# Optimization experiments

Hardware: AMD Instinct MI355X
Metric: run time of the kernel (lower is better)

## Reference

```python
import jax, jax.numpy as jnp
import numpy as np

N_NODES = 50000
N_EDGES = 800000
IN_FEATS = 256
OUT_FEATS = 64


def setup_inputs() -> dict:
    key = jax.random.key(0)
    k1, k2, k3, k4 = jax.random.split(key, 4)
    feat = jax.random.normal(k1, (N_NODES, IN_FEATS), dtype=jnp.float32)
    src = jax.random.randint(k2, (N_EDGES,), 0, N_NODES, dtype=jnp.int32)
    dst = jax.random.randint(k3, (N_EDGES,), 0, N_NODES, dtype=jnp.int32)
    # Glorot-uniform like DGL's GraphConv weight init
    limit = float(np.sqrt(6.0 / (IN_FEATS + OUT_FEATS)))
    W = jax.random.uniform(k4, (IN_FEATS, OUT_FEATS), dtype=jnp.float32,
                           minval=-limit, maxval=limit)
    b = jnp.zeros((OUT_FEATS,), dtype=jnp.float32)
    return {"feat": feat, "src": src, "dst": dst, "W": W, "b": b}


def reference(feat, src, dst, W, b):
    n = feat.shape[0]
    ones = jnp.ones_like(src, dtype=feat.dtype)
    out_deg = jax.ops.segment_sum(ones, src, num_segments=n)
    in_deg = jax.ops.segment_sum(ones, dst, num_segments=n)
    # norm='both': deg^{-1/2}, degrees clamped to min 1 (allow_zero_in_degree)
    norm_src = jax.lax.rsqrt(jnp.maximum(out_deg, 1.0))   # [N]
    norm_dst = jax.lax.rsqrt(jnp.maximum(in_deg, 1.0))    # [N]
    # in_feats > out_feats -> apply weight before aggregation (DGL fast path)
    h = (feat * norm_src[:, None]) @ W                    # [N, out]
    agg = jax.ops.segment_sum(h[src], dst, num_segments=n)  # SpMM: sum messages at dst
    rst = agg * norm_dst[:, None] + b
    return jax.nn.sigmoid(rst)
```

## Files before the change

### kernel.cpp

```cpp
#include <hip/hip_runtime.h>
#include <hip/hip_bf16.h>
#include <math.h>

#define N_NODES 50000
#define N_EDGES 800000
#define IN_F 256
#define OUT_F 64

#define BKT 256
#define NB 196
#define CAP 6144
#define PARTA_BLOCKS 400
#define EPB (N_EDGES / PARTA_BLOCKS)
#define GEMM_BM 32

typedef __attribute__((ext_vector_type(8))) short bf16x8;
typedef __attribute__((ext_vector_type(4))) float f32x4;

__device__ __forceinline__ ushort f2bf(float x) {
    __hip_bfloat16 b = __float2bfloat16(x);
    return *reinterpret_cast<ushort*>(&b);
}
__device__ __forceinline__ float bf_lo(uint v) { return __uint_as_float(v << 16); }
__device__ __forceinline__ float bf_hi(uint v) { return __uint_as_float(v & 0xffff0000u); }

__global__ __launch_bounds__(256) void prep_kernel(int* __restrict__ bcnt,
                                                   const float* __restrict__ W,
                                                   ushort* __restrict__ Wpk) {
    const int tid = threadIdx.x;
    if (blockIdx.x == 0) {
        for (int i = tid; i < 2 * NB; i += 256) bcnt[i] = 0;
    } else {
        const int gid = (blockIdx.x - 1) * 256 + tid;
        const int lane = gid & 63;
        const int ct = (gid >> 6) & 3;
        const int step = gid >> 8;
        const int kg = lane >> 4;
        const int n = lane & 15;
        const float* base = W + (size_t)(step * 32 + kg * 8) * OUT_F + ct * 16 + n;
        union { ushort u[8]; uint4 v; } pk;
        #pragma unroll
        for (int j = 0; j < 8; ++j) pk.u[j] = f2bf(base[(size_t)j * OUT_F]);
        ((uint4*)Wpk)[gid] = pk.v;
    }
}

__global__ __launch_bounds__(512) void partA_kernel(const int* __restrict__ src,
                                                    const int* __restrict__ dst,
                                                    int* __restrict__ bcntD,
                                                    int* __restrict__ bcntS,
                                                    uint* __restrict__ pairsD,
                                                    ushort* __restrict__ srcloc) {
    __shared__ int2 ed[EPB];
    __shared__ uint stgD[EPB];
    __shared__ ushort stgS[EPB];
    __shared__ int lcntD[256], lcntS[256];
    __shared__ int ldofD[256], ldofS[256];
    __shared__ int lbaseD[NB], lbaseS[NB];
    __shared__ int wtotD[4], wtotS[4];
    const int tid = threadIdx.x;
    const int n4 = EPB / 4;

    for (int i = tid; i < 256; i += 512) { lcntD[i] = 0; lcntS[i] = 0; }
    __syncthreads();

    const int4* t4 = (const int4*)(dst + (size_t)blockIdx.x * EPB);
    const int4* s4 = (const int4*)(src + (size_t)blockIdx.x * EPB);
    for (int i = tid; i < n4; i += 512) {
        const int4 d = t4[i];
        const int4 s = s4[i];
        ed[4 * i + 0] = (int2){d.x, s.x};
        ed[4 * i + 1] = (int2){d.y, s.y};
        ed[4 * i + 2] = (int2){d.z, s.z};
        ed[4 * i + 3] = (int2){d.w, s.w};
        atomicAdd(&lcntD[d.x >> 8], 1); atomicAdd(&lcntS[s.x >> 8], 1);
        atomicAdd(&lcntD[d.y >> 8], 1); atomicAdd(&lcntS[s.y >> 8], 1);
        atomicAdd(&lcntD[d.z >> 8], 1); atomicAdd(&lcntS[s.z >> 8], 1);
        atomicAdd(&lcntD[d.w >> 8], 1); atomicAdd(&lcntS[s.w >> 8], 1);
    }
    __syncthreads();

    for (int i = tid; i < NB; i += 512) {
        const int cD = lcntD[i];
        lbaseD[i] = cD ? atomicAdd(&bcntD[i], cD) : 0;
        const int cS = lcntS[i];
        lbaseS[i] = cS ? atomicAdd(&bcntS[i], cS) : 0;
    }

    if (tid < 256) {
        const int lane = tid & 63;
        const int wave = tid >> 6;
        const int vD = lcntD[tid], vS = lcntS[tid];
        int iD = vD, iS = vS;
        #pragma unroll
        for (int d = 1; d < 64; d <<= 1) {
            const int uD = __shfl_up(iD, d, 64);
            const int uS = __shfl_up(iS, d, 64);
            if (lane >= d) { iD += uD; iS += uS; }
        }
        if (lane == 63) { wtotD[wave] = iD; wtotS[wave] = iS; }
        ldofD[tid] = iD - vD;
        ldofS[tid] = iS - vS;
    }
    __syncthreads();
    if (tid < 256) {
        const int wave = tid >> 6;
        int woD = 0, woS = 0;
        #pragma unroll
        for (int w = 0; w < 4; ++w)
            if (w < wave) { woD += wtotD[w]; woS += wtotS[w]; }
        ldofD[tid] += woD;
        ldofS[tid] += woS;
        lcntD[tid] = 0;
        lcntS[tid] = 0;
    }
    __syncthreads();

    for (int i = tid; i < EPB; i += 512) {
        const int2 e = ed[i];
        int bx = e.x >> 8;
        int pos = atomicAdd(&lcntD[bx], 1);
        stgD[ldofD[bx] + pos] =
            ((uint)bx << 24) | ((uint)(e.x & 255) << 16) | (uint)e.y;
        bx = e.y >> 8;
        pos = atomicAdd(&lcntS[bx], 1);
        stgS[ldofS[bx] + pos] = (ushort)((bx << 8) | (e.y & 255));
    }
    __syncthreads();

    for (int i = tid; i < EPB; i += 512) {
        const uint pv = stgD[i];
        const int bD = (int)(pv >> 24);
        pairsD[(size_t)bD * CAP + lbaseD[bD] + (i - ldofD[bD])] = pv & 0xFFFFFFu;
        const ushort sv = stgS[i];
        const int bS = sv >> 8;
        srcloc[(size_t)bS * CAP + lbaseS[bS] + (i - ldofS[bS])] = (ushort)(sv & 255u);
    }
}

__global__ __launch_bounds__(1024) void bucket_kernel(const ushort* __restrict__ srcloc,
                                                      const int* __restrict__ bcntS,
                                                      float* __restrict__ normS,
                                                      const uint* __restrict__ pairsD,
                                                      const int* __restrict__ bcntD,
                                                      uint* __restrict__ ptrdeg,
                                                      ushort* __restrict__ sorted_src) {
    __shared__ int cnt[BKT];
    __shared__ int loff[BKT];
    __shared__ int wtot[4];
    const int bb = blockIdx.x;
    const int tid = threadIdx.x;
    const int node = bb * BKT + tid;

    if (tid < BKT) cnt[tid] = 0;
    __syncthreads();
    const int nS = bcntS[bb];
    const ushort* sp = srcloc + (size_t)bb * CAP;
    for (int i = tid; i < nS; i += 1024) atomicAdd(&cnt[sp[i]], 1);
    __syncthreads();
    if (tid < BKT && node < N_NODES)
        normS[node] = rsqrtf(fmaxf((float)cnt[tid], 1.0f));
    __syncthreads();

    if (tid < BKT) cnt[tid] = 0;
    __syncthreads();
    const int nD = bcntD[bb];
    const uint* pb = pairsD + (size_t)bb * CAP;
    for (int i = tid; i < nD; i += 1024) atomicAdd(&cnt[(pb[i] >> 16) & 255u], 1);
    __syncthreads();

    if (tid < BKT) {
        const int lane = tid & 63;
        const int wave = tid >> 6;
        const int v = cnt[tid];
        int incl = v;
        #pragma unroll
        for (int d = 1; d < 64; d <<= 1) {
            int u = __shfl_up(incl, d, 64);
            if (lane >= d) incl += u;
        }
        if (lane == 63) wtot[wave] = incl;
        loff[tid] = incl - v;
    }
    __syncthreads();
    if (tid < BKT) {
        const int wave = tid >> 6;
        int woff = 0;
        #pragma unroll
        for (int w = 0; w < 4; ++w)
            if (w < wave) woff += wtot[w];
        const int ex = woff + loff[tid];
        loff[tid] = ex;
        const int v = cnt[tid];
        cnt[tid] = 0;
        if (node < N_NODES)
            ptrdeg[node] = (uint)(bb * CAP + ex) | ((uint)v << 21);
    }
    __syncthreads();

    for (int i = tid; i < nD; i += 1024) {
        const uint p = pb[i];
        const int local = (int)((p >> 16) & 255u);
        const int pos = atomicAdd(&cnt[local], 1);
        sorted_src[(size_t)bb * CAP + loff[local] + pos] = (ushort)(p & 0xFFFFu);
    }
}

__global__ __launch_bounds__(256) void gemm_kernel(const float* __restrict__ feat,
                                                   const ushort* __restrict__ Wpk,
                                                   const float* __restrict__ normS,
                                                   ushort* __restrict__ h) {
    __shared__ float ftile[GEMM_BM * IN_F];
    const int tid = threadIdx.x;
    const int lane = tid & 63;
    const int wave = tid >> 6;
    const int m = lane & 15;
    const int g = lane >> 4;
    const int rowBase = blockIdx.x * GEMM_BM;
    const char* fb = (const char*)feat;

    #pragma unroll
    for (int it = 0; it < 8; ++it) {
        const int R = it * 4 + wave;
        const int off = (lane * 16) ^ ((R & 7) << 4);
        int grow = rowBase + R;
        if (grow >= N_NODES) grow = N_NODES - 1;
        __builtin_amdgcn_global_load_lds(
            (const __attribute__((address_space(1))) void*)(fb + ((size_t)grow << 10) + off),
            (__attribute__((address_space(3))) void*)((char*)ftile + it * 4096 + wave * 1024),
            16, 0, 0);
    }
    __syncthreads();

    const int rowHalf = wave & 1;
    const int colHalf = wave >> 1;

    f32x4 acc[2];
    acc[0] = (f32x4){0.f, 0.f, 0.f, 0.f};
    acc[1] = (f32x4){0.f, 0.f, 0.f, 0.f};

    const int Rr = rowHalf * 16 + m;
    const int swz = (Rr & 7) << 4;
    const char* rowb = (const char*)ftile + (Rr << 10);
    const bf16x8* wp = (const bf16x8*)Wpk;

    #pragma unroll
    for (int step = 0; step < 8; ++step) {
        const int kb = step * 128 + g * 32;
        const float4 a0 = *(const float4*)(rowb + (kb ^ swz));
        const float4 a1 = *(const float4*)(rowb + ((kb + 16) ^ swz));
        bf16x8 aa;
        aa[0] = (short)f2bf(a0.x); aa[1] = (short)f2bf(a0.y);
        aa[2] = (short)f2bf(a0.z); aa[3] = (short)f2bf(a0.w);
        aa[4] = (short)f2bf(a1.x); aa[5] = (short)f2bf(a1.y);
        aa[6] = (short)f2bf(a1.z); aa[7] = (short)f2bf(a1.w);
        #pragma unroll
        for (int ct = 0; ct < 2; ++ct)
            acc[ct] = __builtin_amdgcn_mfma_f32_16x16x32_bf16(
                aa, wp[(step * 4 + colHalf * 2 + ct) * 64 + lane], acc[ct], 0, 0, 0);
    }

    #pragma unroll
    for (int j = 0; j < 4; ++j) {
        const int row = rowBase + rowHalf * 16 + g * 4 + j;
        if (row < N_NODES) {
            const float ns = normS[row];
            #pragma unroll
            for (int ct = 0; ct < 2; ++ct)
                h[(size_t)row * OUT_F + colHalf * 32 + ct * 16 + m] =
                    f2bf(acc[ct][j] * ns);
        }
    }
}

__global__ __launch_bounds__(256) void gather_kernel(const uint* __restrict__ ptrdeg,
                                                     const ushort* __restrict__ sorted_src,
                                                     const ushort* __restrict__ h,
                                                     const float* __restrict__ b,
                                                     float* __restrict__ out) {
    const int lane = threadIdx.x & 63;
    const int q = lane & 15;
    const int g = lane >> 4;
    int nid = (int)((blockIdx.x * (size_t)blockDim.x + threadIdx.x) >> 6);
    if (nid >= N_NODES) return;
    nid = __builtin_amdgcn_readfirstlane(nid);

    const uint pd = ptrdeg[nid];
    const int beg = (int)(pd & 0x1FFFFFu);
    const int deg = (int)(pd >> 21);

    float a0 = 0.f, a1 = 0.f, a2 = 0.f, a3 = 0.f;
    const int nfull = deg >> 2;
    int e = beg + g;
    #pragma unroll 4
    for (int i = 0; i < nfull; ++i) {
        const int s = (int)sorted_src[e];
        e += 4;
        const uint2 v = *(const uint2*)(h + (size_t)s * OUT_F + q * 4);
        a0 += bf_lo(v.x); a1 += bf_hi(v.x);
        a2 += bf_lo(v.y); a3 += bf_hi(v.y);
    }
    const int rem = deg & 3;
    if (g < rem) {
        const int s = (int)sorted_src[beg + (deg & ~3) + g];
        const uint2 v = *(const uint2*)(h + (size_t)s * OUT_F + q * 4);
        a0 += bf_lo(v.x); a1 += bf_hi(v.x);
        a2 += bf_lo(v.y); a3 += bf_hi(v.y);
    }
    a0 += __shfl_xor(a0, 16, 64); a1 += __shfl_xor(a1, 16, 64);
    a2 += __shfl_xor(a2, 16, 64); a3 += __shfl_xor(a3, 16, 64);
    a0 += __shfl_xor(a0, 32, 64); a1 += __shfl_xor(a1, 32, 64);
    a2 += __shfl_xor(a2, 32, 64); a3 += __shfl_xor(a3, 32, 64);

    if (g == 0) {
        const float norm = rsqrtf(fmaxf((float)deg, 1.0f));
        const float4 bb = *(const float4*)(b + q * 4);
        float4 o;
        o.x = 1.0f / (1.0f + expf(-(a0 * norm + bb.x)));
        o.y = 1.0f / (1.0f + expf(-(a1 * norm + bb.y)));
        o.z = 1.0f / (1.0f + expf(-(a2 * norm + bb.z)));
        o.w = 1.0f / (1.0f + expf(-(a3 * norm + bb.w)));
        *(float4*)(out + (size_t)nid * OUT_F + q * 4) = o;
    }
}

extern "C" void kernel_launch(void* const* d_in, const int* in_sizes, int n_in,
                              void* d_out, int out_size, void* d_ws, size_t ws_size,
                              hipStream_t stream) {
    const float* feat = (const float*)d_in[0];
    const int* src    = (const int*)d_in[1];
    const int* dst    = (const int*)d_in[2];
    const float* W    = (const float*)d_in[3];
    const float* b    = (const float*)d_in[4];
    float* out = (float*)d_out;

    char* ws = (char*)d_ws;
    size_t off = 0;
    ushort* h = (ushort*)(ws + off);        off += (size_t)N_NODES * OUT_F * 2;
    float* normS = (float*)(ws + off);      off += (size_t)N_NODES * 4;
    uint* ptrdeg = (uint*)(ws + off);       off += (size_t)N_NODES * 4;
    int* bcnt = (int*)(ws + off);           off += (size_t)2 * NB * 4;
    ushort* Wpk = (ushort*)(ws + off);      off += (size_t)IN_F * OUT_F * 2;
    uint* pairsD = (uint*)(ws + off);       off += (size_t)NB * CAP * 4;
    ushort* srcloc = (ushort*)(ws + off);   off += (size_t)NB * CAP * 2;
    ushort* sorted_src = (ushort*)(ws + off); off += (size_t)NB * CAP * 2;
    int* bcntD = bcnt;
    int* bcntS = bcnt + NB;

    prep_kernel<<<9, 256, 0, stream>>>(bcnt, W, Wpk);

    partA_kernel<<<PARTA_BLOCKS, 512, 0, stream>>>(src, dst, bcntD, bcntS, pairsD, srcloc);

    bucket_kernel<<<NB, 1024, 0, stream>>>(srcloc, bcntS, normS,
                                           pairsD, bcntD, ptrdeg, sorted_src);

    gemm_kernel<<<(N_NODES + GEMM_BM - 1) / GEMM_BM, 256, 0, stream>>>(feat, Wpk, normS, h);

    gather_kernel<<<(N_NODES * 64 + 255) / 256, 256, 0, stream>>>(
        ptrdeg, sorted_src, h, b, out);
}
```

Baseline: 74.72 us.

## Fuse edge partitioning with GEMM and move source norm into gather

Removes the GEMM's dependency on the source-degree norm by applying normS per edge inside the gather loop instead of scaling h. That frees the GEMM to run in the same launch as the edge-partition pass, using interleaved heterogeneous blocks (odd blocks partition edges, others compute two 32-row GEMM tiles each), so the partitioning and the dense compute can overlap. The cost is an extra normS load and FMA per edge in the gather. The fused kernel also carries a 64KB shared buffer and 512-thread blocks for both roles, which may reduce occupancy.

```diff
diff --git a/kernel.cpp b/kernel.cpp
--- a/kernel.cpp
+++ b/kernel.cpp
@@ -13,6 +13,7 @@
 #define PARTA_BLOCKS 400
 #define EPB (N_EDGES / PARTA_BLOCKS)
 #define GEMM_BM 32
+#define GEMM_BLOCKS 782
 
 typedef __attribute__((ext_vector_type(8))) short bf16x8;
 typedef __attribute__((ext_vector_type(4))) float f32x4;
@@ -45,96 +46,171 @@
     }
 }
 
-__global__ __launch_bounds__(512) void partA_kernel(const int* __restrict__ src,
+__global__ __launch_bounds__(512) void fused_kernel(const int* __restrict__ src,
                                                     const int* __restrict__ dst,
                                                     int* __restrict__ bcntD,
                                                     int* __restrict__ bcntS,
                                                     uint* __restrict__ pairsD,
-                                                    ushort* __restrict__ srcloc) {
-    __shared__ int2 ed[EPB];
-    __shared__ uint stgD[EPB];
-    __shared__ ushort stgS[EPB];
-    __shared__ int lcntD[256], lcntS[256];
-    __shared__ int ldofD[256], ldofS[256];
-    __shared__ int lbaseD[NB], lbaseS[NB];
-    __shared__ int wtotD[4], wtotS[4];
+                                                    ushort* __restrict__ srcloc,
+                                                    const float* __restrict__ feat,
+                                                    const ushort* __restrict__ Wpk,
+                                                    ushort* __restrict__ h) {
+    __shared__ __align__(16) char smem[65536];
+    const int bi = blockIdx.x;
     const int tid = threadIdx.x;
-    const int n4 = EPB / 4;
-
-    for (int i = tid; i < 256; i += 512) { lcntD[i] = 0; lcntS[i] = 0; }
-    __syncthreads();
-
-    const int4* t4 = (const int4*)(dst + (size_t)blockIdx.x * EPB);
-    const int4* s4 = (const int4*)(src + (size_t)blockIdx.x * EPB);
-    for (int i = tid; i < n4; i += 512) {
-        const int4 d = t4[i];
-        const int4 s = s4[i];
-        ed[4 * i + 0] = (int2){d.x, s.x};
-        ed[4 * i + 1] = (int2){d.y, s.y};
-        ed[4 * i + 2] = (int2){d.z, s.z};
-        ed[4 * i + 3] = (int2){d.w, s.w};
-        atomicAdd(&lcntD[d.x >> 8], 1); atomicAdd(&lcntS[s.x >> 8], 1);
-        atomicAdd(&lcntD[d.y >> 8], 1); atomicAdd(&lcntS[s.y >> 8], 1);
-        atomicAdd(&lcntD[d.z >> 8], 1); atomicAdd(&lcntS[s.z >> 8], 1);
-        atomicAdd(&lcntD[d.w >> 8], 1); atomicAdd(&lcntS[s.w >> 8], 1);
-    }
-    __syncthreads();
-
-    for (int i = tid; i < NB; i += 512) {
-        const int cD = lcntD[i];
-        lbaseD[i] = cD ? atomicAdd(&bcntD[i], cD) : 0;
-        const int cS = lcntS[i];
-        lbaseS[i] = cS ? atomicAdd(&bcntS[i], cS) : 0;
-    }
-
-    if (tid < 256) {
-        const int lane = tid & 63;
-        const int wave = tid >> 6;
-        const int vD = lcntD[tid], vS = lcntS[tid];
-        int iD = vD, iS = vS;
-        #pragma unroll
-        for (int d = 1; d < 64; d <<= 1) {
-            const int uD = __shfl_up(iD, d, 64);
-            const int uS = __shfl_up(iS, d, 64);
-            if (lane >= d) { iD += uD; iS += uS; }
-        }
-        if (lane == 63) { wtotD[wave] = iD; wtotS[wave] = iS; }
-        ldofD[tid] = iD - vD;
-        ldofS[tid] = iS - vS;
-    }
-    __syncthreads();
-    if (tid < 256) {
-        const int wave = tid >> 6;
-        int woD = 0, woS = 0;
-        #pragma unroll
-        for (int w = 0; w < 4; ++w)
-            if (w < wave) { woD += wtotD[w]; woS += wtotS[w]; }
-        ldofD[tid] += woD;
-        ldofS[tid] += woS;
-        lcntD[tid] = 0;
-        lcntS[tid] = 0;
-    }
-    __syncthreads();
-
-    for (int i = tid; i < EPB; i += 512) {
-        const int2 e = ed[i];
-        int bx = e.x >> 8;
-        int pos = atomicAdd(&lcntD[bx], 1);
-        stgD[ldofD[bx] + pos] =
-            ((uint)bx << 24) | ((uint)(e.x & 255) << 16) | (uint)e.y;
-        bx = e.y >> 8;
-        pos = atomicAdd(&lcntS[bx], 1);
-        stgS[ldofS[bx] + pos] = (ushort)((bx << 8) | (e.y & 255));
-    }
-    __syncthreads();
-
-    for (int i = tid; i < EPB; i += 512) {
-        const uint pv = stgD[i];
-        const int bD = (int)(pv >> 24);
-        pairsD[(size_t)bD * CAP + lbaseD[bD] + (i - ldofD[bD])] = pv & 0xFFFFFFu;
-        const ushort sv = stgS[i];
-        const int bS = sv >> 8;
-        srcloc[(size_t)bS * CAP + lbaseS[bS] + (i - ldofS[bS])] = (ushort)(sv & 255u);
+
+    if (bi < 2 * PARTA_BLOCKS && (bi & 1)) {
+        int2* ed      = (int2*)smem;
+        uint* stgD    = (uint*)(smem + 16000);
+        int* lcntD    = (int*)(smem + 24000);
+        int* lcntS    = (int*)(smem + 25024);
+        int* ldofD    = (int*)(smem + 26048);
+        int* ldofS    = (int*)(smem + 27072);
+        int* lbaseD   = (int*)(smem + 28096);
+        int* lbaseS   = (int*)(smem + 28880);
+        int* wtotD    = (int*)(smem + 29664);
+        int* wtotS    = (int*)(smem + 29680);
+        ushort* stgS  = (ushort*)(smem + 29696);
+        const int id = bi >> 1;
+        const int n4 = EPB / 4;
+
+        for (int i = tid; i < 256; i += 512) { lcntD[i] = 0; lcntS[i] = 0; }
+        __syncthreads();
+
+        const int4* t4 = (const int4*)(dst + (size_t)id * EPB);
+        const int4* s4 = (const int4*)(src + (size_t)id * EPB);
+        for (int i = tid; i < n4; i += 512) {
+            const int4 d = t4[i];
+            const int4 s = s4[i];
+            ed[4 * i + 0] = (int2){d.x, s.x};
+            ed[4 * i + 1] = (int2){d.y, s.y};
+            ed[4 * i + 2] = (int2){d.z, s.z};
+            ed[4 * i + 3] = (int2){d.w, s.w};
+            atomicAdd(&lcntD[d.x >> 8], 1); atomicAdd(&lcntS[s.x >> 8], 1);
+            atomicAdd(&lcntD[d.y >> 8], 1); atomicAdd(&lcntS[s.y >> 8], 1);
+            atomicAdd(&lcntD[d.z >> 8], 1); atomicAdd(&lcntS[s.z >> 8], 1);
+            atomicAdd(&lcntD[d.w >> 8], 1); atomicAdd(&lcntS[s.w >> 8], 1);
+        }
+        __syncthreads();
+
+        for (int i = tid; i < NB; i += 512) {
+            const int cD = lcntD[i];
+            lbaseD[i] = cD ? atomicAdd(&bcntD[i], cD) : 0;
+            const int cS = lcntS[i];
+            lbaseS[i] = cS ? atomicAdd(&bcntS[i], cS) : 0;
+        }
+
+        if (tid < 256) {
+            const int lane = tid & 63;
+            const int wave = tid >> 6;
+            const int vD = lcntD[tid], vS = lcntS[tid];
+            int iD = vD, iS = vS;
+            #pragma unroll
+            for (int d = 1; d < 64; d <<= 1) {
+                const int uD = __shfl_up(iD, d, 64);
+                const int uS = __shfl_up(iS, d, 64);
+                if (lane >= d) { iD += uD; iS += uS; }
+            }
+            if (lane == 63) { wtotD[wave] = iD; wtotS[wave] = iS; }
+            ldofD[tid] = iD - vD;
+            ldofS[tid] = iS - vS;
+        }
+        __syncthreads();
+        if (tid < 256) {
+            const int wave = tid >> 6;
+            int woD = 0, woS = 0;
+            #pragma unroll
+            for (int w = 0; w < 4; ++w)
+                if (w < wave) { woD += wtotD[w]; woS += wtotS[w]; }
+            ldofD[tid] += woD;
+            ldofS[tid] += woS;
+            lcntD[tid] = 0;
+            lcntS[tid] = 0;
+        }
+        __syncthreads();
+
+        for (int i = tid; i < EPB; i += 512) {
+            const int2 e = ed[i];
+            int bx = e.x >> 8;
+            int pos = atomicAdd(&lcntD[bx], 1);
+            stgD[ldofD[bx] + pos] =
+                ((uint)bx << 24) | ((uint)(e.x & 255) << 16) | (uint)e.y;
+            bx = e.y >> 8;
+            pos = atomicAdd(&lcntS[bx], 1);
+            stgS[ldofS[bx] + pos] = (ushort)((bx << 8) | (e.y & 255));
+        }
+        __syncthreads();
+
+        for (int i = tid; i < EPB; i += 512) {
+            const uint pv = stgD[i];
+            const int bD = (int)(pv >> 24);
+            pairsD[(size_t)bD * CAP + lbaseD[bD] + (i - ldofD[bD])] = pv & 0xFFFFFFu;
+            const ushort sv = stgS[i];
+            const int bS = sv >> 8;
+            srcloc[(size_t)bS * CAP + lbaseS[bS] + (i - ldofS[bS])] = (ushort)(sv & 255u);
+        }
+    } else {
+        const int id = (bi < 2 * PARTA_BLOCKS) ? (bi >> 1) : (bi - PARTA_BLOCKS);
+        const int half = tid >> 8;
+        const int t = tid & 255;
+        const int lane = t & 63;
+        const int wave = t >> 6;
+        const int m = lane & 15;
+        const int g = lane >> 4;
+        const int rowBase = (id * 2 + half) * GEMM_BM;
+        float* ftile = (float*)(smem + (size_t)half * 32768);
+        const char* fb = (const char*)feat;
+
+        #pragma unroll
+        for (int it = 0; it < 8; ++it) {
+            const int R = it * 4 + wave;
+            const int off = (lane * 16) ^ ((R & 7) << 4);
+            int grow = rowBase + R;
+            if (grow >= N_NODES) grow = N_NODES - 1;
+            __builtin_amdgcn_global_load_lds(
+                (const __attribute__((address_space(1))) void*)(fb + ((size_t)grow << 10) + off),
+                (__attribute__((address_space(3))) void*)((char*)ftile + it * 4096 + wave * 1024),
+                16, 0, 0);
+        }
+        __syncthreads();
+
+        const int rowHalf = wave & 1;
+        const int colHalf = wave >> 1;
+
+        f32x4 acc[2];
+        acc[0] = (f32x4){0.f, 0.f, 0.f, 0.f};
+        acc[1] = (f32x4){0.f, 0.f, 0.f, 0.f};
+
+        const int Rr = rowHalf * 16 + m;
+        const int swz = (Rr & 7) << 4;
+        const char* rowb = (const char*)ftile + (Rr << 10);
+        const bf16x8* wp = (const bf16x8*)Wpk;
+
+        #pragma unroll
+        for (int step = 0; step < 8; ++step) {
+            const int kb = step * 128 + g * 32;
+            const float4 a0 = *(const float4*)(rowb + (kb ^ swz));
+            const float4 a1 = *(const float4*)(rowb + ((kb + 16) ^ swz));
+            bf16x8 aa;
+            aa[0] = (short)f2bf(a0.x); aa[1] = (short)f2bf(a0.y);
+            aa[2] = (short)f2bf(a0.z); aa[3] = (short)f2bf(a0.w);
+            aa[4] = (short)f2bf(a1.x); aa[5] = (short)f2bf(a1.y);
+            aa[6] = (short)f2bf(a1.z); aa[7] = (short)f2bf(a1.w);
+            #pragma unroll
+            for (int ct = 0; ct < 2; ++ct)
+                acc[ct] = __builtin_amdgcn_mfma_f32_16x16x32_bf16(
+                    aa, wp[(step * 4 + colHalf * 2 + ct) * 64 + lane], acc[ct], 0, 0, 0);
+        }
+
+        #pragma unroll
+        for (int j = 0; j < 4; ++j) {
+            const int row = rowBase + rowHalf * 16 + g * 4 + j;
+            if (row < N_NODES) {
+                #pragma unroll
+                for (int ct = 0; ct < 2; ++ct)
+                    h[(size_t)row * OUT_F + colHalf * 32 + ct * 16 + m] = f2bf(acc[ct][j]);
+            }
+        }
     }
 }
 
@@ -206,75 +282,9 @@
     }
 }
 
-__global__ __launch_bounds__(256) void gemm_kernel(const float* __restrict__ feat,
-                                                   const ushort* __restrict__ Wpk,
-                                                   const float* __restrict__ normS,
-                                                   ushort* __restrict__ h) {
-    __shared__ float ftile[GEMM_BM * IN_F];
-    const int tid = threadIdx.x;
-    const int lane = tid & 63;
-    const int wave = tid >> 6;
-    const int m = lane & 15;
-    const int g = lane >> 4;
-    const int rowBase = blockIdx.x * GEMM_BM;
-    const char* fb = (const char*)feat;
-
-    #pragma unroll
-    for (int it = 0; it < 8; ++it) {
-        const int R = it * 4 + wave;
-        const int off = (lane * 16) ^ ((R & 7) << 4);
-        int grow = rowBase + R;
-        if (grow >= N_NODES) grow = N_NODES - 1;
-        __builtin_amdgcn_global_load_lds(
-            (const __attribute__((address_space(1))) void*)(fb + ((size_t)grow << 10) + off),
-            (__attribute__((address_space(3))) void*)((char*)ftile + it * 4096 + wave * 1024),
-            16, 0, 0);
-    }
-    __syncthreads();
-
-    const int rowHalf = wave & 1;
-    const int colHalf = wave >> 1;
-
-    f32x4 acc[2];
-    acc[0] = (f32x4){0.f, 0.f, 0.f, 0.f};
-    acc[1] = (f32x4){0.f, 0.f, 0.f, 0.f};
-
-    const int Rr = rowHalf * 16 + m;
-    const int swz = (Rr & 7) << 4;
-    const char* rowb = (const char*)ftile + (Rr << 10);
-    const bf16x8* wp = (const bf16x8*)Wpk;
-
-    #pragma unroll
-    for (int step = 0; step < 8; ++step) {
-        const int kb = step * 128 + g * 32;
-        const float4 a0 = *(const float4*)(rowb + (kb ^ swz));
-        const float4 a1 = *(const float4*)(rowb + ((kb + 16) ^ swz));
-        bf16x8 aa;
-        aa[0] = (short)f2bf(a0.x); aa[1] = (short)f2bf(a0.y);
-        aa[2] = (short)f2bf(a0.z); aa[3] = (short)f2bf(a0.w);
-        aa[4] = (short)f2bf(a1.x); aa[5] = (short)f2bf(a1.y);
-        aa[6] = (short)f2bf(a1.z); aa[7] = (short)f2bf(a1.w);
-        #pragma unroll
-        for (int ct = 0; ct < 2; ++ct)
-            acc[ct] = __builtin_amdgcn_mfma_f32_16x16x32_bf16(
-                aa, wp[(step * 4 + colHalf * 2 + ct) * 64 + lane], acc[ct], 0, 0, 0);
-    }
-
-    #pragma unroll
-    for (int j = 0; j < 4; ++j) {
-        const int row = rowBase + rowHalf * 16 + g * 4 + j;
-        if (row < N_NODES) {
-            const float ns = normS[row];
-            #pragma unroll
-            for (int ct = 0; ct < 2; ++ct)
-                h[(size_t)row * OUT_F + colHalf * 32 + ct * 16 + m] =
-                    f2bf(acc[ct][j] * ns);
-        }
-    }
-}
-
 __global__ __launch_bounds__(256) void gather_kernel(const uint* __restrict__ ptrdeg,
                                                      const ushort* __restrict__ sorted_src,
+                                                     const float* __restrict__ normS,
                                                      const ushort* __restrict__ h,
                                                      const float* __restrict__ b,
                                                      float* __restrict__ out) {
@@ -296,16 +306,18 @@
     for (int i = 0; i < nfull; ++i) {
         const int s = (int)sorted_src[e];
         e += 4;
+        const float ns = normS[s];
         const uint2 v = *(const uint2*)(h + (size_t)s * OUT_F + q * 4);
-        a0 += bf_lo(v.x); a1 += bf_hi(v.x);
-        a2 += bf_lo(v.y); a3 += bf_hi(v.y);
+        a0 = fmaf(ns, bf_lo(v.x), a0); a1 = fmaf(ns, bf_hi(v.x), a1);
+        a2 = fmaf(ns, bf_lo(v.y), a2); a3 = fmaf(ns, bf_hi(v.y), a3);
     }
     const int rem = deg & 3;
     if (g < rem) {
         const int s = (int)sorted_src[beg + (deg & ~3) + g];
+        const float ns = normS[s];
         const uint2 v = *(const uint2*)(h + (size_t)s * OUT_F + q * 4);
-        a0 += bf_lo(v.x); a1 += bf_hi(v.x);
-        a2 += bf_lo(v.y); a3 += bf_hi(v.y);
+        a0 = fmaf(ns, bf_lo(v.x), a0); a1 = fmaf(ns, bf_hi(v.x), a1);
+        a2 = fmaf(ns, bf_lo(v.y), a2); a3 = fmaf(ns, bf_hi(v.y), a3);
     }
     a0 += __shfl_xor(a0, 16, 64); a1 += __shfl_xor(a1, 16, 64);
     a2 += __shfl_xor(a2, 16, 64); a3 += __shfl_xor(a3, 16, 64);
@@ -349,13 +361,12 @@
 
     prep_kernel<<<9, 256, 0, stream>>>(bcnt, W, Wpk);
 
-    partA_kernel<<<PARTA_BLOCKS, 512, 0, stream>>>(src, dst, bcntD, bcntS, pairsD, srcloc);
+    fused_kernel<<<PARTA_BLOCKS + GEMM_BLOCKS, 512, 0, stream>>>(
+        src, dst, bcntD, bcntS, pairsD, srcloc, feat, Wpk, h);
 
     bucket_kernel<<<NB, 1024, 0, stream>>>(srcloc, bcntS, normS,
                                            pairsD, bcntD, ptrdeg, sorted_src);
 
-    gemm_kernel<<<(N_NODES + GEMM_BM - 1) / GEMM_BM, 256, 0, stream>>>(feat, Wpk, normS, h);
-
     gather_kernel<<<(N_NODES * 64 + 255) / 256, 256, 0, stream>>>(
-        ptrdeg, sorted_src, h, b, out);
-}
+        ptrdeg, sorted_src, normS, h, b, out);
+}
```

Result: faster. 68.15 us (-8.8%).
